# Kernel optimization log

Hardware: AMD Instinct MI355X
Metric: run time of the kernel (lower is better)

Reference implementation:

```python
import jax, jax.numpy as jnp
import numpy as np

N = 50000   # nodes
E = 800000  # edges
D = 128     # hidden_dim == input_dim
H = 8       # heads
C = D // H  # per-head dim = 16
ED = 10     # edge_dim
FF = 4 * D  # ffn hidden = 512


def setup_inputs() -> dict:
    key = jax.random.key(0)
    ks = jax.random.split(key, 20)
    s = 0.05
    p = lambda k, shape: (jax.random.normal(k, shape, jnp.float32) * s)
    return {
        "x": jax.random.normal(ks[0], (N, D), jnp.float32),
        "edge_index": jax.random.randint(ks[1], (2, E), 0, N),
        "edge_attr": jax.random.normal(ks[2], (E, ED), jnp.float32),
        # TransformerConv params (PyG): lin_query/key/value have bias, lin_edge no bias,
        # lin_skip has bias, lin_beta no bias
        "Wq": p(ks[3], (D, D)), "bq": jnp.zeros((D,), jnp.float32),
        "Wk": p(ks[4], (D, D)), "bk": jnp.zeros((D,), jnp.float32),
        "Wv": p(ks[5], (D, D)), "bv": jnp.zeros((D,), jnp.float32),
        "We": p(ks[6], (ED, D)),
        "Wskip": p(ks[7], (D, D)), "bskip": jnp.zeros((D,), jnp.float32),
        "Wbeta": p(ks[8], (3 * D, 1)),
        # GraphNorm params
        "gn_w": jnp.ones((D,), jnp.float32),
        "gn_b": jnp.zeros((D,), jnp.float32),
        "gn_ms": jnp.ones((D,), jnp.float32),  # mean_scale
        # FFN params
        "W1": p(ks[9], (D, FF)), "b1": jnp.zeros((FF,), jnp.float32),
        "W2": p(ks[10], (FF, D)), "b2": jnp.zeros((D,), jnp.float32),
    }


def _layer(x, edge_index, edge_attr, Wq, bq, Wk, bk, Wv, bv, We, Wskip, bskip,
           Wbeta, gn_w, gn_b, gn_ms, W1, b1, W2, b2):
    n = x.shape[0]
    src, dst = edge_index[0], edge_index[1]
    # ---- TransformerConv (concat heads, edge-conditioned, beta skip) ----
    q = (x @ Wq + bq).reshape(n, H, C)
    k = (x @ Wk + bk).reshape(n, H, C)
    v = (x @ Wv + bv).reshape(n, H, C)
    e = (edge_attr @ We).reshape(-1, H, C)          # [E,H,C]
    k_j = k[src] + e                                 # gather + edge bias
    alpha = jnp.einsum('ehc,ehc->eh', q[dst], k_j) / jnp.sqrt(jnp.float32(C))
    # segment softmax over incoming edges of each target node
    amax = jax.ops.segment_max(alpha, dst, num_segments=n)      # [N,H]
    ex = jnp.exp(alpha - amax[dst])
    denom = jax.ops.segment_sum(ex, dst, num_segments=n)        # [N,H]
    alpha = ex / (denom[dst] + 1e-16)
    msg = (v[src] + e) * alpha[:, :, None]           # [E,H,C]
    out = jax.ops.segment_sum(msg.reshape(-1, H * C), dst, num_segments=n)  # [N,D]
    # beta-gated root skip
    x_r = x @ Wskip + bskip
    beta = jax.nn.sigmoid(jnp.concatenate([out, x_r, out - x_r], axis=-1) @ Wbeta)
    x_att = beta * x_r + (1.0 - beta) * out
    # ---- residual + GraphNorm (single graph) ----
    h = x + x_att
    mean = h.mean(axis=0)
    hc = h - gn_ms * mean
    var = (hc * hc).mean(axis=0)
    h = hc / jnp.sqrt(var + 1e-5) * gn_w + gn_b
    # ---- FFN with residual (GELU exact, matching torch default) ----
    ffn = jax.nn.gelu(h @ W1 + b1, approximate=False) @ W2 + b2
    return h + ffn


def reference(x, edge_index, edge_attr, Wq, bq, Wk, bk, Wv, bv, We, Wskip,
              bskip, Wbeta, gn_w, gn_b, gn_ms, W1, b1, W2, b2):
    return _layer(x, edge_index, edge_attr, Wq, bq, Wk, bk, Wv, bv, We, Wskip,
                  bskip, Wbeta, gn_w, gn_b, gn_ms, W1, b1, W2, b2)
```

## Files before the change

kernel.cpp:

```cpp
#include <hip/hip_runtime.h>
#include <hip/hip_fp16.h>
#include <math.h>

#define D 128
#define ED 10
#define FF 512
#define TPAD 520
#define XPAD 136

typedef __attribute__((ext_vector_type(4))) float f32x4;
typedef __attribute__((ext_vector_type(8))) short bf16x8;
using h2 = decltype(__builtin_amdgcn_cvt_pkrtz(0.f, 0.f));
typedef __attribute__((ext_vector_type(2))) float f32x2;

__device__ __forceinline__ ushort f2bf(float f) {
  unsigned u = __float_as_uint(f);
  unsigned r = u + 0x7fffu + ((u >> 16) & 1u);
  return (ushort)(r >> 16);
}
__device__ __forceinline__ float bf2f(ushort u) {
  return __uint_as_float(((unsigned)u) << 16);
}

__device__ __forceinline__ float dpp_add_xor1(float x) {
  int y = __builtin_amdgcn_update_dpp(0, __builtin_bit_cast(int, x), 0xB1, 0xF, 0xF, true);
  return x + __builtin_bit_cast(float, y);
}
__device__ __forceinline__ float dpp_add_xor2(float x) {
  int y = __builtin_amdgcn_update_dpp(0, __builtin_bit_cast(int, x), 0x4E, 0xF, 0xF, true);
  return x + __builtin_bit_cast(float, y);
}

#if __has_builtin(__builtin_amdgcn_cvt_pk_f32_fp8) && __has_builtin(__builtin_amdgcn_cvt_pk_fp8_f32)
#define FP8_HW 1
#else
#define FP8_HW 0
#endif

__device__ __forceinline__ unsigned sw_f2fp8(float f) {
  unsigned u = __float_as_uint(f);
  unsigned s = (u >> 24) & 0x80;
  int e = (int)((u >> 23) & 0xff) - 127;
  unsigned mant = u & 0x7fffff;
  if (e < -9) return s;
  if (e > 8) return s | 0x7e;
  if (e >= -6) {
    unsigned m = mant + 0x7ffff + ((mant >> 20) & 1);
    if (m >= 0x800000) { m = 0; ++e; if (e > 8) return s | 0x7e; }
    return s | ((unsigned)(e + 7) << 3) | (m >> 20);
  }
  unsigned full = 0x800000 | mant;
  int shift = 20 + (-6 - e);
  unsigned m = (full + (1u << (shift - 1)) + ((full >> shift) & 1)) >> shift;
  if (m >= 8) return s | 0x08;
  return s | m;
}
__device__ __forceinline__ float sw_fp82f(unsigned b) {
  unsigned s = (b & 0x80) << 24;
  unsigned e = (b >> 3) & 0xf;
  unsigned m = b & 7;
  if (e == 0) {
    if (m == 0) return __uint_as_float(s);
    float v = (float)(int)m * 0.001953125f;
    return (b & 0x80) ? -v : v;
  }
  return __uint_as_float(s | ((e + 120) << 23) | (m << 20));
}

__device__ __forceinline__ ushort pack_fp8_pair(float a, float b) {
#if FP8_HW
  int r = __builtin_amdgcn_cvt_pk_fp8_f32(a, b, 0, false);
  return (ushort)(r & 0xffff);
#else
  return (ushort)(sw_f2fp8(a) | (sw_f2fp8(b) << 8));
#endif
}
template <bool HI>
__device__ __forceinline__ f32x2 unpack_fp8_pair(unsigned w) {
#if FP8_HW
  auto r = __builtin_amdgcn_cvt_pk_f32_fp8((int)w, HI);
  f32x2 o; o[0] = r[0]; o[1] = r[1];
  return o;
#else
  unsigned v = HI ? (w >> 16) : w;
  f32x2 o; o[0] = sw_fp82f(v & 0xff); o[1] = sw_fp82f((v >> 8) & 0xff);
  return o;
#endif
}

__global__ void prep_hist(const float* __restrict__ Wq, const float* __restrict__ Wk,
                          const float* __restrict__ Wv, const float* __restrict__ Wskip,
                          const float* __restrict__ bq, const float* __restrict__ bk,
                          const float* __restrict__ bv, const float* __restrict__ bskip,
                          const float* __restrict__ W1, const float* __restrict__ W2,
                          const int* __restrict__ dst, int* __restrict__ deg,
                          int* __restrict__ rank, int E,
                          ushort* __restrict__ Wcat_t, float* __restrict__ bcat,
                          ushort* __restrict__ W1t, ushort* __restrict__ W2t) {
  int b = blockIdx.x;
  if (b >= 256) {
    int t = (b - 256) * 256 + threadIdx.x;
    if (t < E) rank[t] = atomicAdd(&deg[dst[t]], 1);
    return;
  }
  int t = b * 256 + threadIdx.x;
  {
    int w = t >> 14, c = (t >> 7) & 127, kk = t & 127;
    const float* W = (w == 0) ? Wq : (w == 1) ? Wk : (w == 2) ? Wv : Wskip;
    Wcat_t[t] = f2bf(W[kk * D + c]);
  }
  {
    int f = t >> 7, kk = t & 127;
    W1t[t] = f2bf(W1[kk * FF + f]);
  }
  {
    int c = t >> 9, f = t & 511;
    W2t[t] = f2bf(W2[f * D + c]);
  }
  if (t < 4 * D) {
    int w = t >> 7;
    const float* bb = (w == 0) ? bq : (w == 1) ? bk : (w == 2) ? bv : bskip;
    bcat[t] = bb[t & 127];
  }
}

__global__ __launch_bounds__(1024) void scan_kernel(const int* __restrict__ deg,
                                                    int* __restrict__ off, int n) {
  __shared__ int part[1024];
  int t = threadIdx.x;
  int chunk = (n + 1023) / 1024;
  int lo = t * chunk, hi = min(lo + chunk, n);
  int s = 0;
  for (int i = lo; i < hi; ++i) s += deg[i];
  part[t] = s;
  __syncthreads();
  for (int dd = 1; dd < 1024; dd <<= 1) {
    int v = (t >= dd) ? part[t - dd] : 0;
    __syncthreads();
    part[t] += v;
    __syncthreads();
  }
  int excl = (t == 0) ? 0 : part[t - 1];
  for (int i = lo; i < hi; ++i) {
    off[i] = excl;
    excl += deg[i];
  }
  if (t == 1023) off[n] = part[1023];
}

__global__ __launch_bounds__(256) void gemm_scatter(
    const float* __restrict__ x, const ushort* __restrict__ Wcat_t,
    const float* __restrict__ bcat, ushort* __restrict__ qb, unsigned* __restrict__ kvf8,
    float* __restrict__ xr, int n, int gm,
    const int* __restrict__ dst, const int* __restrict__ src, const int* __restrict__ rank,
    const int* __restrict__ off, const float* __restrict__ attr, int* __restrict__ srcs,
    unsigned* __restrict__ attrh, int E) {
  if ((int)blockIdx.x >= gm) {
    int t = ((int)blockIdx.x - gm) * 256 + threadIdx.x;
    if (t < E) {
      int pos = off[dst[t]] + rank[t];
      srcs[pos] = src[t];
      const float2* ap = reinterpret_cast<const float2*>(attr + (size_t)t * ED);
#pragma unroll
      for (int j = 0; j < 5; ++j) {
        float2 av = ap[j];
        h2 hh = __builtin_amdgcn_cvt_pkrtz(av.x, av.y);
        attrh[(size_t)pos * 5 + j] = __builtin_bit_cast(unsigned, hh);
      }
    }
    return;
  }
  __shared__ ushort xa[32 * XPAD];
  int r0 = blockIdx.x * 32;
  {
    int row = threadIdx.x >> 3;
    int seg = threadIdx.x & 7;
    int grow = min(r0 + row, n - 1);
    const float4* p = reinterpret_cast<const float4*>(x + (size_t)grow * D + seg * 16);
    float4 f0 = p[0], f1 = p[1], f2 = p[2], f3 = p[3];
    bf16x8 u0, u1;
    u0[0] = (short)f2bf(f0.x); u0[1] = (short)f2bf(f0.y);
    u0[2] = (short)f2bf(f0.z); u0[3] = (short)f2bf(f0.w);
    u0[4] = (short)f2bf(f1.x); u0[5] = (short)f2bf(f1.y);
    u0[6] = (short)f2bf(f1.z); u0[7] = (short)f2bf(f1.w);
    u1[0] = (short)f2bf(f2.x); u1[1] = (short)f2bf(f2.y);
    u1[2] = (short)f2bf(f2.z); u1[3] = (short)f2bf(f2.w);
    u1[4] = (short)f2bf(f3.x); u1[5] = (short)f2bf(f3.y);
    u1[6] = (short)f2bf(f3.z); u1[7] = (short)f2bf(f3.w);
    ushort* dl = xa + row * XPAD + seg * 16;
    *reinterpret_cast<bf16x8*>(dl) = u0;
    *reinterpret_cast<bf16x8*>(dl + 8) = u1;
  }
  __syncthreads();
  int wv = threadIdx.x >> 6;
  int l = threadIdx.x & 63;
  int lr = l & 15, lg = l >> 4;
  const ushort* Wt = Wcat_t + wv * D * D;
  f32x4 acc[2][8];
#pragma unroll
  for (int m = 0; m < 2; ++m)
#pragma unroll
    for (int nn = 0; nn < 8; ++nn) acc[m][nn] = (f32x4)0.f;
#pragma unroll
  for (int kb2 = 0; kb2 < 4; ++kb2) {
    int k0 = kb2 * 32 + lg * 8;
    bf16x8 a[2];
#pragma unroll
    for (int m = 0; m < 2; ++m)
      a[m] = *reinterpret_cast<const bf16x8*>(xa + (m * 16 + lr) * XPAD + k0);
    bf16x8 b[8];
#pragma unroll
    for (int nn = 0; nn < 8; ++nn)
      b[nn] = *reinterpret_cast<const bf16x8*>(Wt + (nn * 16 + lr) * D + k0);
#pragma unroll
    for (int m = 0; m < 2; ++m)
#pragma unroll
      for (int nn = 0; nn < 8; ++nn)
        acc[m][nn] = __builtin_amdgcn_mfma_f32_16x16x32_bf16(a[m], b[nn], acc[m][nn], 0, 0, 0);
  }
#pragma unroll
  for (int m = 0; m < 2; ++m)
#pragma unroll
    for (int nn = 0; nn < 8; ++nn) {
      int col = nn * 16 + lr;
      float bb = bcat[wv * D + col];
#pragma unroll
      for (int j = 0; j < 4; ++j) {
        int row = r0 + m * 16 + lg * 4 + j;
        float val = acc[m][nn][j] + bb;
        if (wv == 1 || wv == 2) {
          float partner = __shfl_xor(val, 1, 64);
          if (((lr & 1) == 0) && row < n) {
            ushort us = pack_fp8_pair(val, partner);
            size_t idx = ((size_t)row * 64 + nn * 8 + (lr >> 1)) * 2 + (wv - 1);
            reinterpret_cast<ushort*>(kvf8)[idx] = us;
          }
        } else if (row < n) {
          if (wv == 0) qb[(size_t)row * D + col] = f2bf(val);
          else xr[(size_t)row * D + col] = val;
        }
      }
    }
}

__global__ __launch_bounds__(256) void node_attn(
    const int* __restrict__ srcs, const int* __restrict__ off,
    const unsigned* __restrict__ attrh, const float* __restrict__ We,
    const ushort* __restrict__ qb, const unsigned* __restrict__ kvf8,
    const float* __restrict__ xr, const float* __restrict__ x,
    const float* __restrict__ Wbeta, float* __restrict__ h,
    float* __restrict__ sums, int n) {
  __shared__ uint4 attrS4[4][64];
  __shared__ unsigned attrS1[4][64];
  __shared__ float rs_h[4 * D], rs_h2[4 * D];
  int wid = threadIdx.x >> 6;
  int l = threadIdx.x & 63;
  int d0 = 2 * l;
  h2 wA[5], wB[5];
#pragma unroll
  for (int t = 0; t < 5; ++t) {
    wA[t] = __builtin_amdgcn_cvt_pkrtz(We[(2 * t) * D + d0], We[(2 * t + 1) * D + d0]);
    wB[t] = __builtin_amdgcn_cvt_pkrtz(We[(2 * t) * D + d0 + 1], We[(2 * t + 1) * D + d0 + 1]);
  }
  float2 wb0 = *reinterpret_cast<const float2*>(Wbeta + d0);
  float2 wb1 = *reinterpret_cast<const float2*>(Wbeta + D + d0);
  float2 wb2 = *reinterpret_cast<const float2*>(Wbeta + 2 * D + d0);
  float s_h0 = 0.f, s_h20 = 0.f, s_h1 = 0.f, s_h21 = 0.f;
  for (int node = blockIdx.x * 4 + wid; node < n; node += gridDim.x * 4) {
    const ushort2 qu = *reinterpret_cast<const ushort2*>(qb + (size_t)node * D + d0);
    float q0 = bf2f(qu.x) * 0.25f, q1 = bf2f(qu.y) * 0.25f;
    int o0 = off[node], dg = off[node + 1] - o0;
    float m = -1e30f, den = 0.f, acc0 = 0.f, acc1 = 0.f;
    for (int chunk = 0; chunk < dg; chunk += 64) {
      int cnt = min(64, dg - chunk);
      long pos = (long)o0 + chunk + l;
      long pend = (long)o0 + dg - 1;
      if (pos > pend) pos = pend;
      int s_l = srcs[pos];
      {
        const unsigned* ah = attrh + (size_t)pos * 5;
        attrS4[wid][l] = make_uint4(ah[0], ah[1], ah[2], ah[3]);
        attrS1[wid][l] = ah[4];
      }
      auto LD = [&](int idx) -> unsigned {
        int ss = __shfl(s_l, idx & 63, 64);
        return kvf8[(size_t)ss * 64 + l];
      };
      auto PROC = [&](unsigned kvw, int i) {
        uint4 av = attrS4[wid][i];
        unsigned av1 = attrS1[wid][i];
        h2 a0 = __builtin_bit_cast(h2, av.x);
        h2 a1 = __builtin_bit_cast(h2, av.y);
        h2 a2 = __builtin_bit_cast(h2, av.z);
        h2 a3 = __builtin_bit_cast(h2, av.w);
        h2 a4 = __builtin_bit_cast(h2, av1);
        float ec0 = __builtin_amdgcn_fdot2(a0, wA[0], 0.f, false);
        ec0 = __builtin_amdgcn_fdot2(a1, wA[1], ec0, false);
        ec0 = __builtin_amdgcn_fdot2(a2, wA[2], ec0, false);
        ec0 = __builtin_amdgcn_fdot2(a3, wA[3], ec0, false);
        ec0 = __builtin_amdgcn_fdot2(a4, wA[4], ec0, false);
        float ec1 = __builtin_amdgcn_fdot2(a0, wB[0], 0.f, false);
        ec1 = __builtin_amdgcn_fdot2(a1, wB[1], ec1, false);
        ec1 = __builtin_amdgcn_fdot2(a2, wB[2], ec1, false);
        ec1 = __builtin_amdgcn_fdot2(a3, wB[3], ec1, false);
        ec1 = __builtin_amdgcn_fdot2(a4, wB[4], ec1, false);
        f32x2 kf = unpack_fp8_pair<false>(kvw);
        f32x2 vf = unpack_fp8_pair<true>(kvw);
        float kk0 = kf[0] + ec0, kk1 = kf[1] + ec1;
        float vv0 = vf[0] + ec0, vv1 = vf[1] + ec1;
        float p = fmaf(q0, kk0, q1 * kk1);
        p = dpp_add_xor1(p);
        p = dpp_add_xor2(p);
        p += __shfl_xor(p, 4, 8);
        if (__any(p > m + 8.f)) {
          float mn = fmaxf(m, p);
          float sc = __expf(m - mn);
          den *= sc; acc0 *= sc; acc1 *= sc;
          m = mn;
        }
        float ex = __expf(p - m);
        den += ex;
        acc0 = fmaf(ex, vv0, acc0);
        acc1 = fmaf(ex, vv1, acc1);
      };
      unsigned p0 = LD(0), p1 = LD(1), p2 = LD(2), p3 = LD(3),
               p4 = LD(4), p5 = LD(5), p6 = LD(6), p7 = LD(7);
      for (int i = 0; i < cnt; i += 8) {
        unsigned c0 = p0, c1 = p1, c2 = p2, c3 = p3, c4 = p4, c5 = p5, c6 = p6, c7 = p7;
        p0 = LD(i + 8);  p1 = LD(i + 9);  p2 = LD(i + 10); p3 = LD(i + 11);
        p4 = LD(i + 12); p5 = LD(i + 13); p6 = LD(i + 14); p7 = LD(i + 15);
        PROC(c0, i);
        if (i + 1 < cnt) PROC(c1, i + 1);
        if (i + 2 < cnt) PROC(c2, i + 2);
        if (i + 3 < cnt) PROC(c3, i + 3);
        if (i + 4 < cnt) PROC(c4, i + 4);
        if (i + 5 < cnt) PROC(c5, i + 5);
        if (i + 6 < cnt) PROC(c6, i + 6);
        if (i + 7 < cnt) PROC(c7, i + 7);
      }
    }
    float inv = 1.f / (den + 1e-16f);
    float oo0 = acc0 * inv, oo1 = acc1 * inv;
    float2 xr2 = *reinterpret_cast<const float2*>(xr + (size_t)node * D + d0);
    float2 x2 = *reinterpret_cast<const float2*>(x + (size_t)node * D + d0);
    float pb = oo0 * wb0.x + xr2.x * wb1.x + (oo0 - xr2.x) * wb2.x
             + oo1 * wb0.y + xr2.y * wb1.y + (oo1 - xr2.y) * wb2.y;
#pragma unroll
    for (int msk = 1; msk < 64; msk <<= 1) pb += __shfl_xor(pb, msk, 64);
    float beta = 1.f / (1.f + __expf(-pb));
    float h0 = x2.x + beta * xr2.x + (1.f - beta) * oo0;
    float h1 = x2.y + beta * xr2.y + (1.f - beta) * oo1;
    *reinterpret_cast<float2*>(h + (size_t)node * D + d0) = make_float2(h0, h1);
    s_h0 += h0; s_h20 += h0 * h0;
    s_h1 += h1; s_h21 += h1 * h1;
  }
  rs_h[wid * D + d0] = s_h0;   rs_h[wid * D + d0 + 1] = s_h1;
  rs_h2[wid * D + d0] = s_h20; rs_h2[wid * D + d0 + 1] = s_h21;
  __syncthreads();
  if (threadIdx.x < D) {
    int d = threadIdx.x;
    float sh = rs_h[d] + rs_h[D + d] + rs_h[2 * D + d] + rs_h[3 * D + d];
    float sh2 = rs_h2[d] + rs_h2[D + d] + rs_h2[2 * D + d] + rs_h2[3 * D + d];
    atomicAdd(&sums[d], sh);
    atomicAdd(&sums[D + d], sh2);
  }
}

__global__ __launch_bounds__(256) void ffn_fused(
    const float* __restrict__ h, const float* __restrict__ sums,
    const float* __restrict__ gn_w, const float* __restrict__ gn_b,
    const float* __restrict__ gn_ms,
    const ushort* __restrict__ W1t, const float* __restrict__ b1,
    const ushort* __restrict__ W2t, const float* __restrict__ b2,
    float* __restrict__ out, float inv_n, int n) {
  __shared__ ushort xa[32 * XPAD];
  __shared__ ushort tt[32 * TPAD];
  __shared__ float scsh[2 * D];
  if (threadIdx.x < D) {
    int d = threadIdx.x;
    float mean = sums[d] * inv_n;
    float ex2 = sums[D + d] * inv_n;
    float ms = gn_ms[d];
    float var = ex2 - 2.f * ms * mean * mean + ms * ms * mean * mean;
    float inv = 1.f / sqrtf(var + 1e-5f);
    float scale = gn_w[d] * inv;
    scsh[d] = scale;
    scsh[D + d] = gn_b[d] - ms * mean * scale;
  }
  __syncthreads();
  int r0 = blockIdx.x * 32;
  {
    int row = threadIdx.x >> 3;
    int seg = threadIdx.x & 7;
    int grow = min(r0 + row, n - 1);
    const float4* p = reinterpret_cast<const float4*>(h + (size_t)grow * D + seg * 16);
    float4 f0 = p[0], f1 = p[1], f2 = p[2], f3 = p[3];
    const float4* sc = reinterpret_cast<const float4*>(scsh + seg * 16);
    const float4* sh = reinterpret_cast<const float4*>(scsh + D + seg * 16);
    float4 s0 = sc[0], s1 = sc[1], s2 = sc[2], s3 = sc[3];
    float4 t0 = sh[0], t1 = sh[1], t2 = sh[2], t3 = sh[3];
    bf16x8 u0, u1;
    u0[0] = (short)f2bf(f0.x * s0.x + t0.x); u0[1] = (short)f2bf(f0.y * s0.y + t0.y);
    u0[2] = (short)f2bf(f0.z * s0.z + t0.z); u0[3] = (short)f2bf(f0.w * s0.w + t0.w);
    u0[4] = (short)f2bf(f1.x * s1.x + t1.x); u0[5] = (short)f2bf(f1.y * s1.y + t1.y);
    u0[6] = (short)f2bf(f1.z * s1.z + t1.z); u0[7] = (short)f2bf(f1.w * s1.w + t1.w);
    u1[0] = (short)f2bf(f2.x * s2.x + t2.x); u1[1] = (short)f2bf(f2.y * s2.y + t2.y);
    u1[2] = (short)f2bf(f2.z * s2.z + t2.z); u1[3] = (short)f2bf(f2.w * s2.w + t2.w);
    u1[4] = (short)f2bf(f3.x * s3.x + t3.x); u1[5] = (short)f2bf(f3.y * s3.y + t3.y);
    u1[6] = (short)f2bf(f3.z * s3.z + t3.z); u1[7] = (short)f2bf(f3.w * s3.w + t3.w);
    ushort* dl = xa + row * XPAD + seg * 16;
    *reinterpret_cast<bf16x8*>(dl) = u0;
    *reinterpret_cast<bf16x8*>(dl + 8) = u1;
  }
  __syncthreads();
  int wv = threadIdx.x >> 6;
  int l = threadIdx.x & 63;
  int lr = l & 15, lg = l >> 4;
  int c0 = wv * 128;
  {
    f32x4 acc[2][8];
#pragma unroll
    for (int m = 0; m < 2; ++m)
#pragma unroll
      for (int nn = 0; nn < 8; ++nn) acc[m][nn] = (f32x4)0.f;
#pragma unroll
    for (int kb = 0; kb < 4; ++kb) {
      int k0 = kb * 32 + lg * 8;
      bf16x8 a[2];
#pragma unroll
      for (int m = 0; m < 2; ++m)
        a[m] = *reinterpret_cast<const bf16x8*>(xa + (m * 16 + lr) * XPAD + k0);
      bf16x8 b[8];
#pragma unroll
      for (int nn = 0; nn < 8; ++nn)
        b[nn] = *reinterpret_cast<const bf16x8*>(W1t + (c0 + nn * 16 + lr) * D + k0);
#pragma unroll
      for (int m = 0; m < 2; ++m)
#pragma unroll
        for (int nn = 0; nn < 8; ++nn)
          acc[m][nn] = __builtin_amdgcn_mfma_f32_16x16x32_bf16(a[m], b[nn], acc[m][nn], 0, 0, 0);
    }
    const float inv_sqrt2 = 0.70710678118654752440f;
#pragma unroll
    for (int m = 0; m < 2; ++m)
#pragma unroll
      for (int nn = 0; nn < 8; ++nn) {
        int col = c0 + nn * 16 + lr;
        float bb = b1[col];
#pragma unroll
        for (int j = 0; j < 4; ++j) {
          int rowl = m * 16 + lg * 4 + j;
          float val = acc[m][nn][j] + bb;
          val = 0.5f * val * (1.f + erff(val * inv_sqrt2));
          tt[rowl * TPAD + col] = f2bf(val);
        }
      }
  }
  __syncthreads();
  {
    f32x4 acc[2][2];
#pragma unroll
    for (int m = 0; m < 2; ++m)
#pragma unroll
      for (int nn = 0; nn < 2; ++nn) acc[m][nn] = (f32x4)0.f;
#pragma unroll 4
    for (int kb = 0; kb < 16; ++kb) {
      int k0 = kb * 32 + lg * 8;
      bf16x8 a[2];
#pragma unroll
      for (int m = 0; m < 2; ++m)
        a[m] = *reinterpret_cast<const bf16x8*>(tt + (m * 16 + lr) * TPAD + k0);
      bf16x8 b[2];
#pragma unroll
      for (int nn = 0; nn < 2; ++nn)
        b[nn] = *reinterpret_cast<const bf16x8*>(W2t + (wv * 32 + nn * 16 + lr) * FF + k0);
#pragma unroll
      for (int m = 0; m < 2; ++m)
#pragma unroll
        for (int nn = 0; nn < 2; ++nn)
          acc[m][nn] = __builtin_amdgcn_mfma_f32_16x16x32_bf16(a[m], b[nn], acc[m][nn], 0, 0, 0);
    }
#pragma unroll
    for (int m = 0; m < 2; ++m)
#pragma unroll
      for (int nn = 0; nn < 2; ++nn) {
        int col = wv * 32 + nn * 16 + lr;
        float bb = b2[col];
#pragma unroll
        for (int j = 0; j < 4; ++j) {
          int rowl = m * 16 + lg * 4 + j;
          int row = r0 + rowl;
          if (row < n) {
            float hn = bf2f(xa[rowl * XPAD + col]);
            out[(size_t)row * D + col] = hn + acc[m][nn][j] + bb;
          }
        }
      }
  }
}

extern "C" void kernel_launch(void* const* d_in, const int* in_sizes, int n_in,
                              void* d_out, int out_size, void* d_ws, size_t ws_size,
                              hipStream_t stream) {
  const float* x     = (const float*)d_in[0];
  const int*   ei    = (const int*)d_in[1];
  const float* attr  = (const float*)d_in[2];
  const float* Wq    = (const float*)d_in[3];
  const float* bq    = (const float*)d_in[4];
  const float* Wk    = (const float*)d_in[5];
  const float* bk    = (const float*)d_in[6];
  const float* Wv    = (const float*)d_in[7];
  const float* bv    = (const float*)d_in[8];
  const float* We    = (const float*)d_in[9];
  const float* Wskip = (const float*)d_in[10];
  const float* bskip = (const float*)d_in[11];
  const float* Wbeta = (const float*)d_in[12];
  const float* gn_w  = (const float*)d_in[13];
  const float* gn_b  = (const float*)d_in[14];
  const float* gn_ms = (const float*)d_in[15];
  const float* W1    = (const float*)d_in[16];
  const float* b1    = (const float*)d_in[17];
  const float* W2    = (const float*)d_in[18];
  const float* b2    = (const float*)d_in[19];

  const int n = in_sizes[0] / D;
  const int E = in_sizes[1] / 2;
  const int* src = ei;
  const int* dst = ei + E;
  const size_t ND = (size_t)n * D;

  ushort* qb = (ushort*)d_ws;
  unsigned* kvf8 = (unsigned*)(qb + ND);
  float* xr = (float*)(kvf8 + (size_t)n * 64);
  int* deg = (int*)(xr + ND);
  float* sums = (float*)(deg + n);
  int* off = (int*)(sums + 2 * D);
  int* srcs = off + n + 1;
  int* rank = srcs + E;
  unsigned* attrh = (unsigned*)(rank + E);
  ushort* Wcat_t = (ushort*)(attrh + (size_t)E * 5);
  ushort* W1t = Wcat_t + 4 * D * D;
  ushort* W2t = W1t + D * FF;
  float* bcat = (float*)(W2t + FF * D);

  (void)hipMemsetAsync(deg, 0, ((size_t)n + 2 * D) * sizeof(int), stream);

  int ghist = (E + 255) / 256;
  prep_hist<<<256 + ghist, 256, 0, stream>>>(Wq, Wk, Wv, Wskip, bq, bk, bv, bskip, W1, W2,
                                             dst, deg, rank, E, Wcat_t, bcat, W1t, W2t);
  scan_kernel<<<1, 1024, 0, stream>>>(deg, off, n);

  int gm = (n + 31) / 32;
  gemm_scatter<<<gm + ghist, 256, 0, stream>>>(x, Wcat_t, bcat, qb, kvf8, xr, n, gm, dst,
                                               src, rank, off, attr, srcs, attrh, E);

  node_attn<<<2048, 256, 0, stream>>>(srcs, off, attrh, We, qb, kvf8, xr, x, Wbeta,
                                      (float*)d_out, sums, n);

  ffn_fused<<<(n + 31) / 32, 256, 0, stream>>>((const float*)d_out, sums, gn_w, gn_b, gn_ms,
                                               W1t, b1, W2t, b2, (float*)d_out,
                                               1.f / (float)n, n);
}
```

Baseline: 385.6 us.

## Split wavefront into two half-waves each processing alternate edges with 4 channels per lane

The node attention kernel now assigns 32 lanes to the 128 channels (4 per lane) and uses the two half-waves to process even and odd incoming edges in parallel. Each half keeps its own online-softmax state, and the two are merged with cross-half shuffles at the end. This halves the serial edge loop length per node and widens the per-lane gathers to 8 bytes, at the cost of more edge-projection dot products per lane, higher register pressure, and a merge step.

Measured after the change: 389.8 us. About the same (+1.1%).

```diff
diff --git a/kernel.cpp b/kernel.cpp
--- a/kernel.cpp
+++ b/kernel.cpp
@@ -255,22 +255,27 @@
   __shared__ float rs_h[4 * D], rs_h2[4 * D];
   int wid = threadIdx.x >> 6;
   int l = threadIdx.x & 63;
-  int d0 = 2 * l;
-  h2 wA[5], wB[5];
-#pragma unroll
-  for (int t = 0; t < 5; ++t) {
-    wA[t] = __builtin_amdgcn_cvt_pkrtz(We[(2 * t) * D + d0], We[(2 * t + 1) * D + d0]);
-    wB[t] = __builtin_amdgcn_cvt_pkrtz(We[(2 * t) * D + d0 + 1], We[(2 * t + 1) * D + d0 + 1]);
-  }
-  float2 wb0 = *reinterpret_cast<const float2*>(Wbeta + d0);
-  float2 wb1 = *reinterpret_cast<const float2*>(Wbeta + D + d0);
-  float2 wb2 = *reinterpret_cast<const float2*>(Wbeta + 2 * D + d0);
-  float s_h0 = 0.f, s_h20 = 0.f, s_h1 = 0.f, s_h21 = 0.f;
+  int l5 = l & 31;
+  int hb = l >> 5;
+  int d0 = 4 * l5;
+  h2 w4[4][5];
+#pragma unroll
+  for (int j = 0; j < 4; ++j)
+#pragma unroll
+    for (int t = 0; t < 5; ++t)
+      w4[j][t] = __builtin_amdgcn_cvt_pkrtz(We[(2 * t) * D + d0 + j],
+                                            We[(2 * t + 1) * D + d0 + j]);
+  float4 wb0 = *reinterpret_cast<const float4*>(Wbeta + d0);
+  float4 wb1 = *reinterpret_cast<const float4*>(Wbeta + D + d0);
+  float4 wb2 = *reinterpret_cast<const float4*>(Wbeta + 2 * D + d0);
+  float sh_[4] = {0.f, 0.f, 0.f, 0.f}, sh2_[4] = {0.f, 0.f, 0.f, 0.f};
   for (int node = blockIdx.x * 4 + wid; node < n; node += gridDim.x * 4) {
-    const ushort2 qu = *reinterpret_cast<const ushort2*>(qb + (size_t)node * D + d0);
+    ushort4 qu = *reinterpret_cast<const ushort4*>(qb + (size_t)node * D + d0);
     float q0 = bf2f(qu.x) * 0.25f, q1 = bf2f(qu.y) * 0.25f;
+    float q2 = bf2f(qu.z) * 0.25f, q3 = bf2f(qu.w) * 0.25f;
     int o0 = off[node], dg = off[node + 1] - o0;
-    float m = -1e30f, den = 0.f, acc0 = 0.f, acc1 = 0.f;
+    float m = -1e30f, den = 0.f;
+    float a0_ = 0.f, a1_ = 0.f, a2_ = 0.f, a3_ = 0.f;
     for (int chunk = 0; chunk < dg; chunk += 64) {
       int cnt = min(64, dg - chunk);
       long pos = (long)o0 + chunk + l;
@@ -282,80 +287,122 @@
         attrS4[wid][l] = make_uint4(ah[0], ah[1], ah[2], ah[3]);
         attrS1[wid][l] = ah[4];
       }
-      auto LD = [&](int idx) -> unsigned {
-        int ss = __shfl(s_l, idx & 63, 64);
-        return kvf8[(size_t)ss * 64 + l];
+      int nproc = (cnt + 1) >> 1;
+      auto LD = [&](int idx) -> uint2 {
+        int ss = __shfl(s_l, (2 * idx + hb) & 63, 64);
+        return *reinterpret_cast<const uint2*>(kvf8 + (size_t)ss * 64 + 2 * l5);
       };
-      auto PROC = [&](unsigned kvw, int i) {
-        uint4 av = attrS4[wid][i];
-        unsigned av1 = attrS1[wid][i];
-        h2 a0 = __builtin_bit_cast(h2, av.x);
-        h2 a1 = __builtin_bit_cast(h2, av.y);
-        h2 a2 = __builtin_bit_cast(h2, av.z);
-        h2 a3 = __builtin_bit_cast(h2, av.w);
-        h2 a4 = __builtin_bit_cast(h2, av1);
-        float ec0 = __builtin_amdgcn_fdot2(a0, wA[0], 0.f, false);
-        ec0 = __builtin_amdgcn_fdot2(a1, wA[1], ec0, false);
-        ec0 = __builtin_amdgcn_fdot2(a2, wA[2], ec0, false);
-        ec0 = __builtin_amdgcn_fdot2(a3, wA[3], ec0, false);
-        ec0 = __builtin_amdgcn_fdot2(a4, wA[4], ec0, false);
-        float ec1 = __builtin_amdgcn_fdot2(a0, wB[0], 0.f, false);
-        ec1 = __builtin_amdgcn_fdot2(a1, wB[1], ec1, false);
-        ec1 = __builtin_amdgcn_fdot2(a2, wB[2], ec1, false);
-        ec1 = __builtin_amdgcn_fdot2(a3, wB[3], ec1, false);
-        ec1 = __builtin_amdgcn_fdot2(a4, wB[4], ec1, false);
-        f32x2 kf = unpack_fp8_pair<false>(kvw);
-        f32x2 vf = unpack_fp8_pair<true>(kvw);
-        float kk0 = kf[0] + ec0, kk1 = kf[1] + ec1;
-        float vv0 = vf[0] + ec0, vv1 = vf[1] + ec1;
-        float p = fmaf(q0, kk0, q1 * kk1);
+      auto PROC = [&](uint2 kv, int i) {
+        int ei = (2 * i + hb) & 63;
+        bool valid = (2 * i + hb) < cnt;
+        uint4 av = attrS4[wid][ei];
+        unsigned av1 = attrS1[wid][ei];
+        h2 t0 = __builtin_bit_cast(h2, av.x);
+        h2 t1 = __builtin_bit_cast(h2, av.y);
+        h2 t2 = __builtin_bit_cast(h2, av.z);
+        h2 t3 = __builtin_bit_cast(h2, av.w);
+        h2 t4 = __builtin_bit_cast(h2, av1);
+        float ec0 = __builtin_amdgcn_fdot2(t0, w4[0][0], 0.f, false);
+        ec0 = __builtin_amdgcn_fdot2(t1, w4[0][1], ec0, false);
+        ec0 = __builtin_amdgcn_fdot2(t2, w4[0][2], ec0, false);
+        ec0 = __builtin_amdgcn_fdot2(t3, w4[0][3], ec0, false);
+        ec0 = __builtin_amdgcn_fdot2(t4, w4[0][4], ec0, false);
+        float ec1 = __builtin_amdgcn_fdot2(t0, w4[1][0], 0.f, false);
+        ec1 = __builtin_amdgcn_fdot2(t1, w4[1][1], ec1, false);
+        ec1 = __builtin_amdgcn_fdot2(t2, w4[1][2], ec1, false);
+        ec1 = __builtin_amdgcn_fdot2(t3, w4[1][3], ec1, false);
+        ec1 = __builtin_amdgcn_fdot2(t4, w4[1][4], ec1, false);
+        float ec2 = __builtin_amdgcn_fdot2(t0, w4[2][0], 0.f, false);
+        ec2 = __builtin_amdgcn_fdot2(t1, w4[2][1], ec2, false);
+        ec2 = __builtin_amdgcn_fdot2(t2, w4[2][2], ec2, false);
+        ec2 = __builtin_amdgcn_fdot2(t3, w4[2][3], ec2, false);
+        ec2 = __builtin_amdgcn_fdot2(t4, w4[2][4], ec2, false);
+        float ec3 = __builtin_amdgcn_fdot2(t0, w4[3][0], 0.f, false);
+        ec3 = __builtin_amdgcn_fdot2(t1, w4[3][1], ec3, false);
+        ec3 = __builtin_amdgcn_fdot2(t2, w4[3][2], ec3, false);
+        ec3 = __builtin_amdgcn_fdot2(t3, w4[3][3], ec3, false);
+        ec3 = __builtin_amdgcn_fdot2(t4, w4[3][4], ec3, false);
+        f32x2 k01 = unpack_fp8_pair<false>(kv.x);
+        f32x2 k23 = unpack_fp8_pair<false>(kv.y);
+        f32x2 v01 = unpack_fp8_pair<true>(kv.x);
+        f32x2 v23 = unpack_fp8_pair<true>(kv.y);
+        float p = q0 * (k01[0] + ec0);
+        p = fmaf(q1, k01[1] + ec1, p);
+        p = fmaf(q2, k23[0] + ec2, p);
+        p = fmaf(q3, k23[1] + ec3, p);
         p = dpp_add_xor1(p);
         p = dpp_add_xor2(p);
-        p += __shfl_xor(p, 4, 8);
         if (__any(p > m + 8.f)) {
           float mn = fmaxf(m, p);
           float sc = __expf(m - mn);
-          den *= sc; acc0 *= sc; acc1 *= sc;
+          den *= sc; a0_ *= sc; a1_ *= sc; a2_ *= sc; a3_ *= sc;
           m = mn;
         }
-        float ex = __expf(p - m);
+        float ex = valid ? __expf(p - m) : 0.f;
         den += ex;
-        acc0 = fmaf(ex, vv0, acc0);
-        acc1 = fmaf(ex, vv1, acc1);
+        a0_ = fmaf(ex, v01[0] + ec0, a0_);
+        a1_ = fmaf(ex, v01[1] + ec1, a1_);
+        a2_ = fmaf(ex, v23[0] + ec2, a2_);
+        a3_ = fmaf(ex, v23[1] + ec3, a3_);
       };
-      unsigned p0 = LD(0), p1 = LD(1), p2 = LD(2), p3 = LD(3),
-               p4 = LD(4), p5 = LD(5), p6 = LD(6), p7 = LD(7);
-      for (int i = 0; i < cnt; i += 8) {
-        unsigned c0 = p0, c1 = p1, c2 = p2, c3 = p3, c4 = p4, c5 = p5, c6 = p6, c7 = p7;
+      uint2 p0 = LD(0), p1 = LD(1), p2 = LD(2), p3 = LD(3),
+            p4 = LD(4), p5 = LD(5), p6 = LD(6), p7 = LD(7);
+      for (int i = 0; i < nproc; i += 8) {
+        uint2 c0 = p0, c1 = p1, c2 = p2, c3 = p3, c4 = p4, c5 = p5, c6 = p6, c7 = p7;
         p0 = LD(i + 8);  p1 = LD(i + 9);  p2 = LD(i + 10); p3 = LD(i + 11);
         p4 = LD(i + 12); p5 = LD(i + 13); p6 = LD(i + 14); p7 = LD(i + 15);
         PROC(c0, i);
-        if (i + 1 < cnt) PROC(c1, i + 1);
-        if (i + 2 < cnt) PROC(c2, i + 2);
-        if (i + 3 < cnt) PROC(c3, i + 3);
-        if (i + 4 < cnt) PROC(c4, i + 4);
-        if (i + 5 < cnt) PROC(c5, i + 5);
-        if (i + 6 < cnt) PROC(c6, i + 6);
-        if (i + 7 < cnt) PROC(c7, i + 7);
+        if (i + 1 < nproc) PROC(c1, i + 1);
+        if (i + 2 < nproc) PROC(c2, i + 2);
+        if (i + 3 < nproc) PROC(c3, i + 3);
+        if (i + 4 < nproc) PROC(c4, i + 4);
+        if (i + 5 < nproc) PROC(c5, i + 5);
+        if (i + 6 < nproc) PROC(c6, i + 6);
+        if (i + 7 < nproc) PROC(c7, i + 7);
       }
     }
-    float inv = 1.f / (den + 1e-16f);
-    float oo0 = acc0 * inv, oo1 = acc1 * inv;
-    float2 xr2 = *reinterpret_cast<const float2*>(xr + (size_t)node * D + d0);
-    float2 x2 = *reinterpret_cast<const float2*>(x + (size_t)node * D + d0);
-    float pb = oo0 * wb0.x + xr2.x * wb1.x + (oo0 - xr2.x) * wb2.x
-             + oo1 * wb0.y + xr2.y * wb1.y + (oo1 - xr2.y) * wb2.y;
-#pragma unroll
-    for (int msk = 1; msk < 64; msk <<= 1) pb += __shfl_xor(pb, msk, 64);
+    float mB = __shfl_xor(m, 32, 64);
+    float denB = __shfl_xor(den, 32, 64);
+    float b0 = __shfl_xor(a0_, 32, 64);
+    float b1 = __shfl_xor(a1_, 32, 64);
+    float b2 = __shfl_xor(a2_, 32, 64);
+    float b3 = __shfl_xor(a3_, 32, 64);
+    float mT = fmaxf(m, mB);
+    float sA = __expf(m - mT), sB = __expf(mB - mT);
+    float denT = den * sA + denB * sB;
+    float inv = 1.f / (denT + 1e-16f);
+    float oo0 = (a0_ * sA + b0 * sB) * inv;
+    float oo1 = (a1_ * sA + b1 * sB) * inv;
+    float oo2 = (a2_ * sA + b2 * sB) * inv;
+    float oo3 = (a3_ * sA + b3 * sB) * inv;
+    float4 xr4 = *reinterpret_cast<const float4*>(xr + (size_t)node * D + d0);
+    float4 x4 = *reinterpret_cast<const float4*>(x + (size_t)node * D + d0);
+    float pb = oo0 * wb0.x + xr4.x * wb1.x + (oo0 - xr4.x) * wb2.x
+             + oo1 * wb0.y + xr4.y * wb1.y + (oo1 - xr4.y) * wb2.y
+             + oo2 * wb0.z + xr4.z * wb1.z + (oo2 - xr4.z) * wb2.z
+             + oo3 * wb0.w + xr4.w * wb1.w + (oo3 - xr4.w) * wb2.w;
+#pragma unroll
+    for (int msk = 1; msk < 32; msk <<= 1) pb += __shfl_xor(pb, msk, 32);
     float beta = 1.f / (1.f + __expf(-pb));
-    float h0 = x2.x + beta * xr2.x + (1.f - beta) * oo0;
-    float h1 = x2.y + beta * xr2.y + (1.f - beta) * oo1;
-    *reinterpret_cast<float2*>(h + (size_t)node * D + d0) = make_float2(h0, h1);
-    s_h0 += h0; s_h20 += h0 * h0;
-    s_h1 += h1; s_h21 += h1 * h1;
-  }
-  rs_h[wid * D + d0] = s_h0;   rs_h[wid * D + d0 + 1] = s_h1;
-  rs_h2[wid * D + d0] = s_h20; rs_h2[wid * D + d0 + 1] = s_h21;
+    float h0 = x4.x + beta * xr4.x + (1.f - beta) * oo0;
+    float h1 = x4.y + beta * xr4.y + (1.f - beta) * oo1;
+    float h2_ = x4.z + beta * xr4.z + (1.f - beta) * oo2;
+    float h3 = x4.w + beta * xr4.w + (1.f - beta) * oo3;
+    if (hb == 0) {
+      *reinterpret_cast<float4*>(h + (size_t)node * D + d0) = make_float4(h0, h1, h2_, h3);
+      sh_[0] += h0; sh2_[0] += h0 * h0;
+      sh_[1] += h1; sh2_[1] += h1 * h1;
+      sh_[2] += h2_; sh2_[2] += h2_ * h2_;
+      sh_[3] += h3; sh2_[3] += h3 * h3;
+    }
+  }
+  if (hb == 0) {
+#pragma unroll
+    for (int j = 0; j < 4; ++j) {
+      rs_h[wid * D + d0 + j] = sh_[j];
+      rs_h2[wid * D + d0 + j] = sh2_[j];
+    }
+  }
   __syncthreads();
   if (threadIdx.x < D) {
     int d = threadIdx.x;
```
